# Performance work log

Measured on AMD Instinct MI355X. Metric: run time of the kernel, lower is better.

The kernel has to match this reference:

```python
import jax, jax.numpy as jnp
import numpy as np

B, N, M, F, D = 4, 8, 64, 128, 128
EPS = 1e-5


def setup_inputs() -> dict:
    key = jax.random.key(0)
    ks = jax.random.split(key, 6)
    s1 = 1.0 / np.sqrt(5 * F)
    s2 = 1.0 / np.sqrt(F)
    return {
        "x": jax.random.normal(ks[0], (B, N, M, F), dtype=jnp.float32),
        "W1": jax.random.uniform(ks[1], (F, 5 * F), jnp.float32, -s1, s1),
        "b1": jax.random.uniform(ks[2], (F,), jnp.float32, -s1, s1),
        "gamma": jnp.ones((F,), jnp.float32),
        "beta": jnp.zeros((F,), jnp.float32),
        "bias_p": jax.random.normal(ks[3], (F,), jnp.float32) * 0.02,
        "W2": jax.random.uniform(ks[4], (D, F), jnp.float32, -s2, s2),
        "b2": jax.random.uniform(ks[5], (D,), jnp.float32, -s2, s2),
    }


def reference(x, W1, b1, gamma, beta, bias_p, W2, b2):
    b, n, m, f = x.shape
    e = jnp.eye(m, dtype=x.dtype)[:, :, None]        # (M,M,1) diagonal mask
    xi = x[:, :, :, None, :]                          # value indexed by row i
    xj = x[:, :, None, :, :]                          # value indexed by col j
    mean = jnp.mean(x, axis=2, keepdims=True)[:, :, :, None, :]  # (B,N,1,1,F)
    shp = (b, n, m, m, f)
    # Equivariant 1->2 lift: [diag(x), row-bcast, col-bcast, diag(mean), mean-bcast]
    xAll = jnp.concatenate([
        xi * e,
        jnp.broadcast_to(xi, shp),
        jnp.broadcast_to(xj, shp),
        jnp.broadcast_to(mean * e, shp),
        jnp.broadcast_to(mean, shp),
    ], axis=-1)                                       # (B,N,M,M,5F)
    h = jnp.einsum('bnijk,fk->bnijf', xAll, W1) + b1  # fc1
    mu = jnp.mean(h, axis=-1, keepdims=True)
    var = jnp.mean((h - mu) ** 2, axis=-1, keepdims=True)
    h = (h - mu) / jnp.sqrt(var + EPS) * gamma + beta # LayerNorm
    h = jax.nn.relu(h)
    h = h + bias_p * e                                # diagonal-masked bias
    return jnp.einsum('bnijf,df->bnijd', h, W2) + b2  # fc2 -> (B,N,M,M,D)
```

## Files before the change

### kernel.cpp

```cpp
#include <hip/hip_runtime.h>

typedef __bf16 bf16x4 __attribute__((ext_vector_type(4)));
typedef __bf16 bf16x8 __attribute__((ext_vector_type(8)));
typedef float  f32x4v __attribute__((ext_vector_type(4)));

#define HS 136


__global__ __launch_bounds__(256) void k1_prep(
    const float* __restrict__ x, const float* __restrict__ W1,
    const float* __restrict__ b1, const float* __restrict__ W2,
    float* __restrict__ Up, float* __restrict__ V, float* __restrict__ Dg,
    __bf16* __restrict__ W2b)
{
  __shared__ __align__(16) __bf16 Xhi[64 * HS];
  __shared__ __align__(16) __bf16 Xlo[64 * HS];
  __shared__ float msum[128], pm[256], mw[128];

  const int tid  = threadIdx.x;
  const int bn   = blockIdx.x / 6;
  const int ch   = blockIdx.x % 6;
  const int lane = tid & 63;
  const int w    = tid >> 6;
  const int pidx = ch >> 1;

  if (tid < 128) msum[tid] = 0.f;
  __syncthreads();

  {
    const float4* xv = reinterpret_cast<const float4*>(x + (size_t)bn * 8192);
    const int c = tid & 31;
    float4 ps = {0.f, 0.f, 0.f, 0.f};
#pragma unroll
    for (int it = 0; it < 8; ++it) {
      int p = tid + 256 * it;
      int r = p >> 5;
      float4 v = xv[p];
      ps.x += v.x; ps.y += v.y; ps.z += v.z; ps.w += v.w;
      bf16x4 hv, lv;
      hv[0] = (__bf16)v.x; lv[0] = (__bf16)(v.x - (float)hv[0]);
      hv[1] = (__bf16)v.y; lv[1] = (__bf16)(v.y - (float)hv[1]);
      hv[2] = (__bf16)v.z; lv[2] = (__bf16)(v.z - (float)hv[2]);
      hv[3] = (__bf16)v.w; lv[3] = (__bf16)(v.w - (float)hv[3]);
      *reinterpret_cast<bf16x4*>(&Xhi[r * HS + 4 * c]) = hv;
      *reinterpret_cast<bf16x4*>(&Xlo[r * HS + 4 * c]) = lv;
    }
    atomicAdd(&msum[4 * c + 0], ps.x);
    atomicAdd(&msum[4 * c + 1], ps.y);
    atomicAdd(&msum[4 * c + 2], ps.z);
    atomicAdd(&msum[4 * c + 3], ps.w);
  }

  if (ch == 4) {
    const float4* w2v = reinterpret_cast<const float4*>(W2);
#pragma unroll
    for (int it = 0; it < 16; ++it) {
      int p = tid + 256 * it;
      float4 v = w2v[p];
      bf16x4 hv;
      hv[0] = (__bf16)v.x; hv[1] = (__bf16)v.y;
      hv[2] = (__bf16)v.z; hv[3] = (__bf16)v.w;
      reinterpret_cast<bf16x4*>(W2b)[p] = hv;
    }
  }
  __syncthreads();

  {
    const int f  = tid & 127;
    const int hh = tid >> 7;
    float acc = 0.f;
    if (pidx < 2) {
      const float4* wv4 = reinterpret_cast<const float4*>(
          W1 + (size_t)f * 640 + (pidx == 0 ? 384 : 512) + hh * 64);
#pragma unroll
      for (int kc = 0; kc < 16; ++kc) {
        float4 wv = wv4[kc];
        int k = hh * 64 + 4 * kc;
        acc += msum[k] * wv.x + msum[k + 1] * wv.y +
               msum[k + 2] * wv.z + msum[k + 3] * wv.w;
      }
    }
    pm[tid] = acc;
  }
  __syncthreads();
  if (tid < 128)
    mw[tid] = (pm[tid] + pm[tid + 128]) * (1.f / 64.f) +
              (pidx == 1 ? b1[tid] : 0.f);
  __syncthreads();

  const int m    = lane & 15;
  const int quad = lane >> 4;
  bf16x8 ahi[4], alo[4];
#pragma unroll
  for (int ks = 0; ks < 4; ++ks) {
    ahi[ks] = *reinterpret_cast<const bf16x8*>(&Xhi[(16 * w + m) * HS + 32 * ks + 8 * quad]);
    alo[ks] = *reinterpret_cast<const bf16x8*>(&Xlo[(16 * w + m) * HS + 32 * ks + 8 * quad]);
  }

  float* rout = (pidx == 0) ? Dg : (pidx == 1 ? Up : V);
#pragma unroll
  for (int tt = 0; tt < 4; ++tt) {
    const int fout = (((4 * ch + tt) & 7) * 16) + m;
    const float* wrow = W1 + (size_t)fout * 640 + pidx * 128;
    f32x4v a = {0.f, 0.f, 0.f, 0.f};
#pragma unroll
    for (int ks = 0; ks < 4; ++ks) {
      float4 w0 = *reinterpret_cast<const float4*>(wrow + 32 * ks + 8 * quad);
      float4 w1 = *reinterpret_cast<const float4*>(wrow + 32 * ks + 8 * quad + 4);
      bf16x8 bhi, blo;
      bhi[0] = (__bf16)w0.x; blo[0] = (__bf16)(w0.x - (float)bhi[0]);
      bhi[1] = (__bf16)w0.y; blo[1] = (__bf16)(w0.y - (float)bhi[1]);
      bhi[2] = (__bf16)w0.z; blo[2] = (__bf16)(w0.z - (float)bhi[2]);
      bhi[3] = (__bf16)w0.w; blo[3] = (__bf16)(w0.w - (float)bhi[3]);
      bhi[4] = (__bf16)w1.x; blo[4] = (__bf16)(w1.x - (float)bhi[4]);
      bhi[5] = (__bf16)w1.y; blo[5] = (__bf16)(w1.y - (float)bhi[5]);
      bhi[6] = (__bf16)w1.z; blo[6] = (__bf16)(w1.z - (float)bhi[6]);
      bhi[7] = (__bf16)w1.w; blo[7] = (__bf16)(w1.w - (float)bhi[7]);
      a = __builtin_amdgcn_mfma_f32_16x16x32_bf16(ahi[ks], bhi, a, 0, 0, 0);
      a = __builtin_amdgcn_mfma_f32_16x16x32_bf16(alo[ks], bhi, a, 0, 0, 0);
      a = __builtin_amdgcn_mfma_f32_16x16x32_bf16(ahi[ks], blo, a, 0, 0, 0);
    }
    const float addv = mw[fout];
#pragma unroll
    for (int rg = 0; rg < 4; ++rg) {
      int ii = 16 * w + 4 * quad + rg;
      rout[((size_t)bn * 64 + ii) * 128 + fout] = a[rg] + addv;
    }
  }
}

__global__ __launch_bounds__(256) void k2_main(
    const float* __restrict__ Up, const float* __restrict__ V,
    const float* __restrict__ Dg, const __bf16* __restrict__ W2b,
    const float* __restrict__ gamma, const float* __restrict__ beta,
    const float* __restrict__ bias_p, const float* __restrict__ b2,
    float* __restrict__ out)
{
  __shared__ __align__(16) __bf16 W2s[128 * HS];
  __shared__ __align__(16) __bf16 Hs[64 * HS];

  const int tid  = threadIdx.x;
  const int bid  = blockIdx.x;
  const int bn   = bid >> 6;
  const int i    = bid & 63;
  const int lane = tid & 63;
  const int w    = tid >> 6;

  {
    const uint4* w2v = reinterpret_cast<const uint4*>(W2b);
#pragma unroll
    for (int it = 0; it < 8; ++it) {
      int p   = tid + 256 * it;
      int row = p >> 4;
      int col = (p & 15) * 8;
      *reinterpret_cast<uint4*>(&W2s[row * HS + col]) = w2v[p];
    }
  }

  {
    const int c    = lane & 31;
    const int half = lane >> 5;
    const size_t base = (size_t)bn * 64;
    const float4 up4 = reinterpret_cast<const float4*>(Up + (base + i) * 128)[c];
    const float4 dg4 = reinterpret_cast<const float4*>(Dg + (base + i) * 128)[c];
    const float4 g4  = reinterpret_cast<const float4*>(gamma)[c];
    const float4 be4 = reinterpret_cast<const float4*>(beta)[c];
    const float4 bp4 = reinterpret_cast<const float4*>(bias_p)[c];
    float4 v4s[8];
#pragma unroll
    for (int it = 0; it < 8; ++it) {
      int r = 8 * it + 2 * w + half;
      v4s[it] = reinterpret_cast<const float4*>(V + (base + r) * 128)[c];
    }
#pragma unroll
    for (int it = 0; it < 8; ++it) {
      int r = 8 * it + 2 * w + half;
      float4 v4 = v4s[it];
      float h0 = v4.x + up4.x, h1 = v4.y + up4.y;
      float h2 = v4.z + up4.z, h3 = v4.w + up4.w;
      if (r == i) { h0 += dg4.x; h1 += dg4.y; h2 += dg4.z; h3 += dg4.w; }
      float s = h0 + h1 + h2 + h3;
      float q = h0 * h0 + h1 * h1 + h2 * h2 + h3 * h3;
#pragma unroll
      for (int off = 16; off > 0; off >>= 1) {
        s += __shfl_xor(s, off, 32);
        q += __shfl_xor(q, off, 32);
      }
      float mu   = s * (1.f / 128.f);
      float var  = q * (1.f / 128.f) - mu * mu;
      float rstd = rsqrtf(var + 1e-5f);
      h0 = fmaxf(fmaf((h0 - mu) * rstd, g4.x, be4.x), 0.f);
      h1 = fmaxf(fmaf((h1 - mu) * rstd, g4.y, be4.y), 0.f);
      h2 = fmaxf(fmaf((h2 - mu) * rstd, g4.z, be4.z), 0.f);
      h3 = fmaxf(fmaf((h3 - mu) * rstd, g4.w, be4.w), 0.f);
      if (r == i) { h0 += bp4.x; h1 += bp4.y; h2 += bp4.z; h3 += bp4.w; }
      bf16x4 hv;
      hv[0] = (__bf16)h0; hv[1] = (__bf16)h1;
      hv[2] = (__bf16)h2; hv[3] = (__bf16)h3;
      *reinterpret_cast<bf16x4*>(&Hs[r * HS + 4 * c]) = hv;
    }
  }
  __syncthreads();

  const int m    = lane & 15;
  const int quad = lane >> 4;
  bf16x8 bh[4];
#pragma unroll
  for (int ks = 0; ks < 4; ++ks)
    bh[ks] = *reinterpret_cast<const bf16x8*>(
        &Hs[(16 * w + m) * HS + 32 * ks + 8 * quad]);

  const size_t obase = (size_t)bid * 8192;
  float* orow = out + obase + (size_t)(16 * w + m) * 128;
#pragma unroll
  for (int t = 0; t < 8; ++t) {
    f32x4v a = {0.f, 0.f, 0.f, 0.f};
#pragma unroll
    for (int ks = 0; ks < 4; ++ks) {
      bf16x8 aw = *reinterpret_cast<const bf16x8*>(
          &W2s[(16 * t + m) * HS + 32 * ks + 8 * quad]);
      a = __builtin_amdgcn_mfma_f32_16x16x32_bf16(aw, bh[ks], a, 0, 0, 0);
    }
    const float4 b2v = *reinterpret_cast<const float4*>(b2 + 16 * t + 4 * quad);
    float4 o;
    o.x = a[0] + b2v.x; o.y = a[1] + b2v.y;
    o.z = a[2] + b2v.z; o.w = a[3] + b2v.w;
    *reinterpret_cast<float4*>(orow + 16 * t + 4 * quad) = o;
  }
}

extern "C" void kernel_launch(void* const* d_in, const int* in_sizes, int n_in,
                              void* d_out, int out_size, void* d_ws, size_t ws_size,
                              hipStream_t stream) {
  const float* x      = (const float*)d_in[0];
  const float* W1     = (const float*)d_in[1];
  const float* b1     = (const float*)d_in[2];
  const float* gamma  = (const float*)d_in[3];
  const float* beta   = (const float*)d_in[4];
  const float* bias_p = (const float*)d_in[5];
  const float* W2     = (const float*)d_in[6];
  const float* b2     = (const float*)d_in[7];

  float*  Up  = (float*)d_ws;
  float*  V   = Up + 2048 * 128;
  float*  Dg  = V + 2048 * 128;
  __bf16* W2b = (__bf16*)(Dg + 2048 * 128);

  k1_prep<<<192, 256, 0, stream>>>(x, W1, b1, W2, Up, V, Dg, W2b);
  k2_main<<<2048, 256, 0, stream>>>(Up, V, Dg, W2b, gamma, beta, bias_p, b2,
                                    (float*)d_out);
}
```

Before: 113.7 us.

## Precompute LayerNorm stats via algebraic decomposition and build H fragments in registers

Adds a stats kernel that derives per-(i,j) LayerNorm mean and rstd algebraically from row sums, sums of squares and a U·V^T dot product computed with split-bf16 MFMA, with the diagonal handled exactly. The main kernel then reads mu/rstd and builds the bf16 H operand straight into MFMA registers, dropping the shuffle reductions and the shared-memory H staging. This costs an extra kernel launch and workspace traffic for the Mu/Rs tables, and the variance comes from E[h^2]-mu^2 with a bf16-split dot product, which may lose precision.

```diff
diff --git a/kernel.cpp b/kernel.cpp
--- a/kernel.cpp
+++ b/kernel.cpp
@@ -129,15 +129,153 @@
   }
 }
 
+__global__ __launch_bounds__(256) void k1b_stats(
+    const float* __restrict__ Up, const float* __restrict__ V,
+    const float* __restrict__ Dg, float* __restrict__ Mu,
+    float* __restrict__ Rs)
+{
+  __shared__ __align__(16) __bf16 Vhi[64 * HS];
+  __shared__ __align__(16) __bf16 Vlo[64 * HS];
+  __shared__ __align__(16) __bf16 Uhi[16 * HS];
+  __shared__ __align__(16) __bf16 Ulo[16 * HS];
+  __shared__ float SVs[64], PVs[64], SUs[16], PUs[16], dmus[16], drss[16];
+
+  const int tid  = threadIdx.x;
+  const int bn   = blockIdx.x >> 2;
+  const int ig   = blockIdx.x & 3;
+  const int lane = tid & 63;
+  const int w    = tid >> 6;
+
+  const float* Vb = V  + (size_t)bn * 8192;
+  const float* Ub = Up + ((size_t)bn * 64 + 16 * ig) * 128;
+  const float* Db = Dg + ((size_t)bn * 64 + 16 * ig) * 128;
+
+  {
+    const float4* vv = reinterpret_cast<const float4*>(Vb);
+#pragma unroll
+    for (int it = 0; it < 8; ++it) {
+      int p = tid + 256 * it;
+      int r = p >> 5, c = p & 31;
+      float4 v = vv[p];
+      bf16x4 hv, lv;
+      hv[0] = (__bf16)v.x; lv[0] = (__bf16)(v.x - (float)hv[0]);
+      hv[1] = (__bf16)v.y; lv[1] = (__bf16)(v.y - (float)hv[1]);
+      hv[2] = (__bf16)v.z; lv[2] = (__bf16)(v.z - (float)hv[2]);
+      hv[3] = (__bf16)v.w; lv[3] = (__bf16)(v.w - (float)hv[3]);
+      *reinterpret_cast<bf16x4*>(&Vhi[r * HS + 4 * c]) = hv;
+      *reinterpret_cast<bf16x4*>(&Vlo[r * HS + 4 * c]) = lv;
+    }
+    const float4* uv = reinterpret_cast<const float4*>(Ub);
+#pragma unroll
+    for (int it = 0; it < 2; ++it) {
+      int p = tid + 256 * it;
+      int r = p >> 5, c = p & 31;
+      float4 v = uv[p];
+      bf16x4 hv, lv;
+      hv[0] = (__bf16)v.x; lv[0] = (__bf16)(v.x - (float)hv[0]);
+      hv[1] = (__bf16)v.y; lv[1] = (__bf16)(v.y - (float)hv[1]);
+      hv[2] = (__bf16)v.z; lv[2] = (__bf16)(v.z - (float)hv[2]);
+      hv[3] = (__bf16)v.w; lv[3] = (__bf16)(v.w - (float)hv[3]);
+      *reinterpret_cast<bf16x4*>(&Uhi[r * HS + 4 * c]) = hv;
+      *reinterpret_cast<bf16x4*>(&Ulo[r * HS + 4 * c]) = lv;
+    }
+  }
+
+  {
+    const int hw = tid >> 5;
+    const int c  = tid & 31;
+#pragma unroll
+    for (int it = 0; it < 8; ++it) {
+      int r = 8 * it + hw;
+      float4 v = reinterpret_cast<const float4*>(Vb + (size_t)r * 128)[c];
+      float s = v.x + v.y + v.z + v.w;
+      float q = v.x * v.x + v.y * v.y + v.z * v.z + v.w * v.w;
+#pragma unroll
+      for (int off = 16; off > 0; off >>= 1) {
+        s += __shfl_xor(s, off, 32);
+        q += __shfl_xor(q, off, 32);
+      }
+      if (c == 0) { SVs[r] = s; PVs[r] = q; }
+    }
+#pragma unroll
+    for (int it = 0; it < 2; ++it) {
+      int r = 8 * it + hw;
+      float4 u = reinterpret_cast<const float4*>(Ub + (size_t)r * 128)[c];
+      float s = u.x + u.y + u.z + u.w;
+      float q = u.x * u.x + u.y * u.y + u.z * u.z + u.w * u.w;
+#pragma unroll
+      for (int off = 16; off > 0; off >>= 1) {
+        s += __shfl_xor(s, off, 32);
+        q += __shfl_xor(q, off, 32);
+      }
+      if (c == 0) { SUs[r] = s; PUs[r] = q; }
+    }
+#pragma unroll
+    for (int it = 0; it < 2; ++it) {
+      int r  = 8 * it + hw;
+      int gi = 16 * ig + r;
+      float4 u = reinterpret_cast<const float4*>(Ub + (size_t)r * 128)[c];
+      float4 d = reinterpret_cast<const float4*>(Db + (size_t)r * 128)[c];
+      float4 v = reinterpret_cast<const float4*>(Vb + (size_t)gi * 128)[c];
+      float h0 = u.x + d.x + v.x, h1 = u.y + d.y + v.y;
+      float h2 = u.z + d.z + v.z, h3 = u.w + d.w + v.w;
+      float s = h0 + h1 + h2 + h3;
+      float q = h0 * h0 + h1 * h1 + h2 * h2 + h3 * h3;
+#pragma unroll
+      for (int off = 16; off > 0; off >>= 1) {
+        s += __shfl_xor(s, off, 32);
+        q += __shfl_xor(q, off, 32);
+      }
+      if (c == 0) {
+        float mu  = s * (1.f / 128.f);
+        float var = q * (1.f / 128.f) - mu * mu;
+        dmus[r] = mu;
+        drss[r] = rsqrtf(var + 1e-5f);
+      }
+    }
+  }
+  __syncthreads();
+
+  const int m    = lane & 15;
+  const int quad = lane >> 4;
+  f32x4v a = {0.f, 0.f, 0.f, 0.f};
+#pragma unroll
+  for (int ks = 0; ks < 4; ++ks) {
+    bf16x8 vah = *reinterpret_cast<const bf16x8*>(&Vhi[(16 * w + m) * HS + 32 * ks + 8 * quad]);
+    bf16x8 val = *reinterpret_cast<const bf16x8*>(&Vlo[(16 * w + m) * HS + 32 * ks + 8 * quad]);
+    bf16x8 ubh = *reinterpret_cast<const bf16x8*>(&Uhi[m * HS + 32 * ks + 8 * quad]);
+    bf16x8 ubl = *reinterpret_cast<const bf16x8*>(&Ulo[m * HS + 32 * ks + 8 * quad]);
+    a = __builtin_amdgcn_mfma_f32_16x16x32_bf16(vah, ubh, a, 0, 0, 0);
+    a = __builtin_amdgcn_mfma_f32_16x16x32_bf16(val, ubh, a, 0, 0, 0);
+    a = __builtin_amdgcn_mfma_f32_16x16x32_bf16(vah, ubl, a, 0, 0, 0);
+  }
+
+  const int i  = 16 * ig + m;
+  const float su = SUs[m], pu = PUs[m];
+  float* mrow = Mu + ((size_t)bn * 64 + i) * 64;
+  float* rrow = Rs + ((size_t)bn * 64 + i) * 64;
+#pragma unroll
+  for (int rg = 0; rg < 4; ++rg) {
+    int j = 16 * w + 4 * quad + rg;
+    float mu  = (su + SVs[j]) * (1.f / 128.f);
+    float q   = pu + PVs[j] + 2.f * a[rg];
+    float var = q * (1.f / 128.f) - mu * mu;
+    float rstd = rsqrtf(var + 1e-5f);
+    if (w == ig && (4 * quad + rg) == m) { mu = dmus[m]; rstd = drss[m]; }
+    mrow[j] = mu;
+    rrow[j] = rstd;
+  }
+}
+
 __global__ __launch_bounds__(256) void k2_main(
     const float* __restrict__ Up, const float* __restrict__ V,
     const float* __restrict__ Dg, const __bf16* __restrict__ W2b,
+    const float* __restrict__ Mu, const float* __restrict__ Rs,
     const float* __restrict__ gamma, const float* __restrict__ beta,
     const float* __restrict__ bias_p, const float* __restrict__ b2,
     float* __restrict__ out)
 {
   __shared__ __align__(16) __bf16 W2s[128 * HS];
-  __shared__ __align__(16) __bf16 Hs[64 * HS];
 
   const int tid  = threadIdx.x;
   const int bid  = blockIdx.x;
@@ -145,6 +283,8 @@
   const int i    = bid & 63;
   const int lane = tid & 63;
   const int w    = tid >> 6;
+  const int m    = lane & 15;
+  const int quad = lane >> 4;
 
   {
     const uint4* w2v = reinterpret_cast<const uint4*>(W2b);
@@ -157,61 +297,56 @@
     }
   }
 
-  {
-    const int c    = lane & 31;
-    const int half = lane >> 5;
-    const size_t base = (size_t)bn * 64;
-    const float4 up4 = reinterpret_cast<const float4*>(Up + (base + i) * 128)[c];
-    const float4 dg4 = reinterpret_cast<const float4*>(Dg + (base + i) * 128)[c];
-    const float4 g4  = reinterpret_cast<const float4*>(gamma)[c];
-    const float4 be4 = reinterpret_cast<const float4*>(beta)[c];
-    const float4 bp4 = reinterpret_cast<const float4*>(bias_p)[c];
-    float4 v4s[8];
-#pragma unroll
-    for (int it = 0; it < 8; ++it) {
-      int r = 8 * it + 2 * w + half;
-      v4s[it] = reinterpret_cast<const float4*>(V + (base + r) * 128)[c];
-    }
-#pragma unroll
-    for (int it = 0; it < 8; ++it) {
-      int r = 8 * it + 2 * w + half;
-      float4 v4 = v4s[it];
-      float h0 = v4.x + up4.x, h1 = v4.y + up4.y;
-      float h2 = v4.z + up4.z, h3 = v4.w + up4.w;
-      if (r == i) { h0 += dg4.x; h1 += dg4.y; h2 += dg4.z; h3 += dg4.w; }
-      float s = h0 + h1 + h2 + h3;
-      float q = h0 * h0 + h1 * h1 + h2 * h2 + h3 * h3;
-#pragma unroll
-      for (int off = 16; off > 0; off >>= 1) {
-        s += __shfl_xor(s, off, 32);
-        q += __shfl_xor(q, off, 32);
-      }
-      float mu   = s * (1.f / 128.f);
-      float var  = q * (1.f / 128.f) - mu * mu;
-      float rstd = rsqrtf(var + 1e-5f);
-      h0 = fmaxf(fmaf((h0 - mu) * rstd, g4.x, be4.x), 0.f);
-      h1 = fmaxf(fmaf((h1 - mu) * rstd, g4.y, be4.y), 0.f);
-      h2 = fmaxf(fmaf((h2 - mu) * rstd, g4.z, be4.z), 0.f);
-      h3 = fmaxf(fmaf((h3 - mu) * rstd, g4.w, be4.w), 0.f);
-      if (r == i) { h0 += bp4.x; h1 += bp4.y; h2 += bp4.z; h3 += bp4.w; }
-      bf16x4 hv;
-      hv[0] = (__bf16)h0; hv[1] = (__bf16)h1;
-      hv[2] = (__bf16)h2; hv[3] = (__bf16)h3;
-      *reinterpret_cast<bf16x4*>(&Hs[r * HS + 4 * c]) = hv;
-    }
-  }
-  __syncthreads();
-
-  const int m    = lane & 15;
-  const int quad = lane >> 4;
-  bf16x8 bh[4];
-#pragma unroll
-  for (int ks = 0; ks < 4; ++ks)
-    bh[ks] = *reinterpret_cast<const bf16x8*>(
-        &Hs[(16 * w + m) * HS + 32 * ks + 8 * quad]);
+  const int j = 16 * w + m;
+  const size_t base = (size_t)bn * 64;
+  const float mu = Mu[(base + i) * 64 + j];
+  const float rs = Rs[(base + i) * 64 + j];
+  const bool  dia = (j == i);
+  const float* uprow = Up + (base + i) * 128;
+  const float* vrow  = V  + (base + j) * 128;
+  const float* dgrow = Dg + (base + i) * 128;
+
+  bf16x8 hfrag[4];
+#pragma unroll
+  for (int ks = 0; ks < 4; ++ks) {
+    const int c0 = 32 * ks + 8 * quad;
+    float4 u0 = *reinterpret_cast<const float4*>(uprow + c0);
+    float4 u1 = *reinterpret_cast<const float4*>(uprow + c0 + 4);
+    float4 v0 = *reinterpret_cast<const float4*>(vrow + c0);
+    float4 v1 = *reinterpret_cast<const float4*>(vrow + c0 + 4);
+    float h[8] = {u0.x + v0.x, u0.y + v0.y, u0.z + v0.z, u0.w + v0.w,
+                  u1.x + v1.x, u1.y + v1.y, u1.z + v1.z, u1.w + v1.w};
+    if (dia) {
+      float4 d0 = *reinterpret_cast<const float4*>(dgrow + c0);
+      float4 d1 = *reinterpret_cast<const float4*>(dgrow + c0 + 4);
+      h[0] += d0.x; h[1] += d0.y; h[2] += d0.z; h[3] += d0.w;
+      h[4] += d1.x; h[5] += d1.y; h[6] += d1.z; h[7] += d1.w;
+    }
+    float4 g0  = *reinterpret_cast<const float4*>(gamma + c0);
+    float4 g1  = *reinterpret_cast<const float4*>(gamma + c0 + 4);
+    float4 be0 = *reinterpret_cast<const float4*>(beta + c0);
+    float4 be1 = *reinterpret_cast<const float4*>(beta + c0 + 4);
+    float gg[8] = {g0.x, g0.y, g0.z, g0.w, g1.x, g1.y, g1.z, g1.w};
+    float bb[8] = {be0.x, be0.y, be0.z, be0.w, be1.x, be1.y, be1.z, be1.w};
+    float r8[8];
+#pragma unroll
+    for (int e = 0; e < 8; ++e)
+      r8[e] = fmaxf(fmaf((h[e] - mu) * rs, gg[e], bb[e]), 0.f);
+    if (dia) {
+      float4 bp0 = *reinterpret_cast<const float4*>(bias_p + c0);
+      float4 bp1 = *reinterpret_cast<const float4*>(bias_p + c0 + 4);
+      r8[0] += bp0.x; r8[1] += bp0.y; r8[2] += bp0.z; r8[3] += bp0.w;
+      r8[4] += bp1.x; r8[5] += bp1.y; r8[6] += bp1.z; r8[7] += bp1.w;
+    }
+    bf16x8 f;
+#pragma unroll
+    for (int e = 0; e < 8; ++e) f[e] = (__bf16)r8[e];
+    hfrag[ks] = f;
+  }
+  __syncthreads();
 
   const size_t obase = (size_t)bid * 8192;
-  float* orow = out + obase + (size_t)(16 * w + m) * 128;
+  float* orow = out + obase + (size_t)j * 128;
 #pragma unroll
   for (int t = 0; t < 8; ++t) {
     f32x4v a = {0.f, 0.f, 0.f, 0.f};
@@ -219,7 +354,7 @@
     for (int ks = 0; ks < 4; ++ks) {
       bf16x8 aw = *reinterpret_cast<const bf16x8*>(
           &W2s[(16 * t + m) * HS + 32 * ks + 8 * quad]);
-      a = __builtin_amdgcn_mfma_f32_16x16x32_bf16(aw, bh[ks], a, 0, 0, 0);
+      a = __builtin_amdgcn_mfma_f32_16x16x32_bf16(aw, hfrag[ks], a, 0, 0, 0);
     }
     const float4 b2v = *reinterpret_cast<const float4*>(b2 + 16 * t + 4 * quad);
     float4 o;
@@ -245,8 +380,11 @@
   float*  V   = Up + 2048 * 128;
   float*  Dg  = V + 2048 * 128;
   __bf16* W2b = (__bf16*)(Dg + 2048 * 128);
+  float*  Mu  = (float*)(W2b + 16384);
+  float*  Rs  = Mu + 2048 * 64;
 
   k1_prep<<<192, 256, 0, stream>>>(x, W1, b1, W2, Up, V, Dg, W2b);
-  k2_main<<<2048, 256, 0, stream>>>(Up, V, Dg, W2b, gamma, beta, bias_p, b2,
-                                    (float*)d_out);
+  k1b_stats<<<128, 256, 0, stream>>>(Up, V, Dg, Mu, Rs);
+  k2_main<<<2048, 256, 0, stream>>>(Up, V, Dg, W2b, Mu, Rs, gamma, beta,
+                                    bias_p, b2, (float*)d_out);
 }
```

Result: slower. 129.4 us (+13.7%).
